# Performance work log

Measured on AMD Instinct MI355X. Metric: run time of the kernel, lower is better.

The kernel has to match this reference:

```python
import jax, jax.numpy as jnp
import numpy as np
from jax import lax

IMG_H, IMG_W = 800.0, 800.0
REG_WEIGHTS = (10.0, 10.0, 5.0, 5.0)
SCORE_THRESH = 0.05
NMS_THRESH = 0.5
NUM_DETECTIONS = 100
MIN_SIZE = 1.0
BBOX_XFORM_CLIP = float(np.log(1000.0 / 16.0))


def setup_inputs() -> dict:
    key = jax.random.key(0)
    k1, k2, k3, k4 = jax.random.split(key, 4)
    N, C = 1000, 81
    class_logit = jax.random.normal(k1, (N, C), dtype=jnp.float32) * 2.0
    box_regression = jax.random.normal(k2, (N, C * 4), dtype=jnp.float32)
    # proposals: valid (x1,y1,x2,y2) boxes inside the 800x800 image
    ctr = jax.random.uniform(k3, (N, 2), dtype=jnp.float32) * 800.0
    wh = jax.random.uniform(k4, (N, 2), dtype=jnp.float32) * 200.0 + 8.0
    x1y1 = jnp.clip(ctr - 0.5 * wh, 0.0, 800.0)
    x2y2 = jnp.clip(ctr + 0.5 * wh, 0.0, 800.0)
    proposal = jnp.concatenate([x1y1, x2y2], axis=1)
    return dict(class_logit=class_logit, box_regression=box_regression, proposal=proposal)


def decode_boxes(deltas, boxes):
    # deltas: [..., 4] (dx,dy,dw,dh); boxes: [..., 4] (x1,y1,x2,y2)
    wx, wy, ww, wh = REG_WEIGHTS
    widths = boxes[..., 2] - boxes[..., 0]
    heights = boxes[..., 3] - boxes[..., 1]
    ctr_x = boxes[..., 0] + 0.5 * widths
    ctr_y = boxes[..., 1] + 0.5 * heights
    dx = deltas[..., 0] / wx
    dy = deltas[..., 1] / wy
    dw = jnp.minimum(deltas[..., 2] / ww, BBOX_XFORM_CLIP)
    dh = jnp.minimum(deltas[..., 3] / wh, BBOX_XFORM_CLIP)
    pcx = dx * widths + ctr_x
    pcy = dy * heights + ctr_y
    pw = jnp.exp(dw) * widths
    ph = jnp.exp(dh) * heights
    return jnp.stack([pcx - 0.5 * pw, pcy - 0.5 * ph, pcx + 0.5 * pw, pcy + 0.5 * ph], axis=-1)


def pairwise_iou(b):
    # b: [N, 4] -> [N, N]
    area = (b[:, 2] - b[:, 0]) * (b[:, 3] - b[:, 1])
    lt = jnp.maximum(b[:, None, :2], b[None, :, :2])
    rb = jnp.minimum(b[:, None, 2:], b[None, :, 2:])
    wh = jnp.clip(rb - lt, 0.0)
    inter = wh[..., 0] * wh[..., 1]
    return inter / (area[:, None] + area[None, :] - inter + 1e-9)


def nms_one_class(boxes, scores):
    # boxes: [N, 4]; scores: [N] with invalid entries masked to -1.
    # Exact greedy NMS: sort by score desc, suppress IoU > NMS_THRESH.
    N = boxes.shape[0]
    order = jnp.argsort(-scores)
    b = boxes[order]
    s = scores[order]
    iou = pairwise_iou(b)
    valid = s > -0.5

    def body(carry, xs):
        keep, i = carry
        row, v = xs
        suppressed = jnp.any(keep & (row > NMS_THRESH))
        keep = keep.at[i].set(v & jnp.logical_not(suppressed))
        return (keep, i + 1), None

    (keep, _), _ = lax.scan(body, (jnp.zeros((N,), bool), jnp.int32(0)), (iou, valid))
    s_kept = jnp.where(keep, s, -1.0)
    top_s, top_i = lax.top_k(s_kept, NUM_DETECTIONS)  # kept are already score-sorted
    out_valid = top_s > -0.5
    out_boxes = jnp.where(out_valid[:, None], b[top_i], 0.0)
    out_scores = jnp.where(out_valid, top_s, 0.0)
    return out_boxes, out_scores, out_valid


def reference(class_logit, box_regression, proposal):
    N, C = class_logit.shape
    pred_score = jax.nn.softmax(class_logit, axis=-1)           # [N, C]
    deltas = box_regression.reshape(N, C, 4)
    boxes = decode_boxes(deltas[:, 1:, :], proposal[:, None, :])  # [N, C-1, 4]
    # clip to image (process_box)
    boxes = jnp.stack([
        jnp.clip(boxes[..., 0], 0.0, IMG_W),
        jnp.clip(boxes[..., 1], 0.0, IMG_H),
        jnp.clip(boxes[..., 2], 0.0, IMG_W),
        jnp.clip(boxes[..., 3], 0.0, IMG_H),
    ], axis=-1)
    w = boxes[..., 2] - boxes[..., 0]
    h = boxes[..., 3] - boxes[..., 1]
    score_fg = pred_score[:, 1:]                                 # [N, C-1]
    valid = (score_fg >= SCORE_THRESH) & (w >= MIN_SIZE) & (h >= MIN_SIZE)
    scores_m = jnp.where(valid, score_fg, -1.0)
    boxes_c = jnp.transpose(boxes, (1, 0, 2))                    # [C-1, N, 4]
    scores_c = scores_m.T                                        # [C-1, N]
    out_boxes, out_scores, out_valid = jax.vmap(nms_one_class)(boxes_c, scores_c)
    labels = jnp.broadcast_to(jnp.arange(1, C, dtype=jnp.int32)[:, None], out_scores.shape)
    labels = jnp.where(out_valid, labels, 0)
    # padded per-class detections: boxes [C-1, D, 4], scores/labels/valid [C-1, D]
    return out_boxes, out_scores, labels, out_valid
```

## Files before the change

### kernel.cpp

```cpp
#include <hip/hip_runtime.h>
#include <math.h>

#define N_PROP   1000
#define C_ALL    81
#define N_FG     80
#define TOPK     100
#define CAP      1024
#define IMG_WH   800.0f
#define SCORE_TH 0.05f
#define NMS_TH   0.5f
#define MIN_SZ   1.0f
#define BBOX_CLIP 4.135166556742356f

typedef unsigned long long u64;

__global__ __launch_bounds__(256) void softmax_stats_kernel(
    const float* __restrict__ logits,
    float* __restrict__ smax,
    float* __restrict__ ssum)
{
    const int wave = threadIdx.x >> 6;
    const int lane = threadIdx.x & 63;
    const int n = blockIdx.x * 4 + wave;
    if (n >= N_PROP) return;
    const float* row = logits + n * C_ALL;

    float v1 = row[lane];
    float v2 = (lane < C_ALL - 64) ? row[64 + lane] : 0.f;

    float m = (lane < C_ALL - 64) ? fmaxf(v1, v2) : v1;
    #pragma unroll
    for (int off = 32; off >= 1; off >>= 1)
        m = fmaxf(m, __shfl_xor(m, off, 64));

    float s = expf(v1 - m) + ((lane < C_ALL - 64) ? expf(v2 - m) : 0.0f);
    #pragma unroll
    for (int off = 32; off >= 1; off >>= 1)
        s += __shfl_xor(s, off, 64);

    if (lane == 0) { smax[n] = m; ssum[n] = s; }
}

__global__ __launch_bounds__(256) void roihead_kernel(
    const float* __restrict__ logits,
    const float* __restrict__ boxreg,
    const float* __restrict__ prop,
    const float* __restrict__ smax,
    const float* __restrict__ ssum,
    float* __restrict__ out)
{
    __shared__ u64   s_key[CAP];
    __shared__ float cx1[CAP], cy1[CAP], cx2[CAP], cy2[CAP], car[CAP];
    __shared__ float sx1[CAP], sy1[CAP], sx2[CAP], sy2[CAP], sar[CAP];
    __shared__ u64   s_mask[256 * 4];
    __shared__ u64   s_keep[4];
    __shared__ unsigned char s_rem[CAP];
    __shared__ int   s_cnt, s_emit;

    const int c   = blockIdx.x;
    const int tid = threadIdx.x;
    const int col = c + 1;

    const int OFF_SCORES = N_FG * TOPK * 4;
    const int OFF_LABELS = OFF_SCORES + N_FG * TOPK;
    const int OFF_VALID  = OFF_LABELS + N_FG * TOPK;

    for (int t = tid; t < TOPK * 4; t += 256) out[c * TOPK * 4 + t] = 0.0f;
    for (int t = tid; t < TOPK; t += 256) {
        out[OFF_SCORES + c * TOPK + t] = 0.0f;
        out[OFF_LABELS + c * TOPK + t] = 0.0f;
        out[OFF_VALID  + c * TOPK + t] = 0.0f;
    }
    if (tid == 0) { s_cnt = 0; s_emit = 0; }
    __syncthreads();

    for (int n = tid; n < N_PROP; n += 256) {
        float score = expf(logits[n * C_ALL + col] - smax[n]) / ssum[n];

        float4 p = *(const float4*)(prop + n * 4);
        float w  = p.z - p.x;
        float h  = p.w - p.y;
        float pcx0 = p.x + 0.5f * w;
        float pcy0 = p.y + 0.5f * h;

        float4 d = *(const float4*)(boxreg + n * (C_ALL * 4) + col * 4);
        float dx = d.x / 10.0f;
        float dy = d.y / 10.0f;
        float dw = fminf(d.z / 5.0f, BBOX_CLIP);
        float dh = fminf(d.w / 5.0f, BBOX_CLIP);

        float pcx = dx * w + pcx0;
        float pcy = dy * h + pcy0;
        float pw  = expf(dw) * w;
        float ph  = expf(dh) * h;

        float x1 = fminf(fmaxf(pcx - 0.5f * pw, 0.0f), IMG_WH);
        float y1 = fminf(fmaxf(pcy - 0.5f * ph, 0.0f), IMG_WH);
        float x2 = fminf(fmaxf(pcx + 0.5f * pw, 0.0f), IMG_WH);
        float y2 = fminf(fmaxf(pcy + 0.5f * ph, 0.0f), IMG_WH);

        float bw = x2 - x1;
        float bh = y2 - y1;
        if (score >= SCORE_TH && bw >= MIN_SZ && bh >= MIN_SZ) {
            int slot = atomicAdd(&s_cnt, 1);
            unsigned int fb = __float_as_uint(score);
            s_key[slot] = ((u64)fb << 20) | ((u64)(1023 - n) << 10) | (u64)slot;
            cx1[slot] = x1; cy1[slot] = y1; cx2[slot] = x2; cy2[slot] = y2;
            car[slot] = bw * bh;
        }
    }
    __syncthreads();

    const int V = s_cnt;
    if (V == 0) return;

    int VP2 = 1; while (VP2 < V) VP2 <<= 1;
    for (int t = V + tid; t < VP2; t += 256) s_key[t] = 0ull;
    __syncthreads();

    for (int k = 2; k <= VP2; k <<= 1) {
        for (int j = k >> 1; j > 0; j >>= 1) {
            for (int i = tid; i < VP2; i += 256) {
                int ixj = i ^ j;
                if (ixj > i) {
                    u64 a = s_key[i], b = s_key[ixj];
                    bool dir = ((i & k) == 0);
                    if ((b > a) == dir) { s_key[i] = b; s_key[ixj] = a; }
                }
            }
            __syncthreads();
        }
    }

    for (int t = tid; t < V; t += 256) {
        int slot = (int)(s_key[t] & 1023u);
        sx1[t] = cx1[slot]; sy1[t] = cy1[slot];
        sx2[t] = cx2[slot]; sy2[t] = cy2[slot];
        sar[t] = car[slot];
    }
    __syncthreads();

    if (V <= 256) {
        const int BW = (V + 63) >> 6;
        for (int i = tid; i < V; i += 256) {
            float x1i = sx1[i], y1i = sy1[i], x2i = sx2[i], y2i = sy2[i];
            float ai  = sar[i];
            for (int w = 0; w < BW; ++w) {
                u64 mrow = 0;
                int j0 = w << 6;
                int j1 = min(V, j0 + 64);
                for (int j = max(j0, i + 1); j < j1; ++j) {
                    float lx = fmaxf(x1i, sx1[j]);
                    float ly = fmaxf(y1i, sy1[j]);
                    float rx = fminf(x2i, sx2[j]);
                    float ry = fminf(y2i, sy2[j]);
                    float iw = fmaxf(rx - lx, 0.0f);
                    float ih = fmaxf(ry - ly, 0.0f);
                    float inter = iw * ih;
                    float iou = inter / (ai + sar[j] - inter + 1e-9f);
                    if (iou > NMS_TH) mrow |= 1ull << (j - j0);
                }
                s_mask[(i << 2) + w] = mrow;
            }
        }
        __syncthreads();

        if (tid == 0) {
            u64 r0 = 0, r1 = 0, r2 = 0, r3 = 0;
            u64 k0 = 0, k1 = 0, k2 = 0, k3 = 0;
            int kept = 0;
            for (int i = 0; i < V; ++i) {
                int w = i >> 6;
                u64 bit = 1ull << (i & 63);
                u64 rw = (w == 0) ? r0 : (w == 1) ? r1 : (w == 2) ? r2 : r3;
                if (rw & bit) continue;
                if (w == 0) k0 |= bit; else if (w == 1) k1 |= bit;
                else if (w == 2) k2 |= bit; else k3 |= bit;
                if (++kept >= TOPK) break;
                const u64* mr = &s_mask[i << 2];
                r0 |= mr[0];
                if (BW > 1) r1 |= mr[1];
                if (BW > 2) r2 |= mr[2];
                if (BW > 3) r3 |= mr[3];
            }
            s_keep[0] = k0; s_keep[1] = k1; s_keep[2] = k2; s_keep[3] = k3;
        }
        __syncthreads();

        u64 kw0 = s_keep[0], kw1 = s_keep[1], kw2 = s_keep[2], kw3 = s_keep[3];
        for (int t = tid; t < V; t += 256) {
            int w = t >> 6;
            u64 kw = (w == 0) ? kw0 : (w == 1) ? kw1 : (w == 2) ? kw2 : kw3;
            if (!((kw >> (t & 63)) & 1ull)) continue;
            int rank = 0;
            if (w > 0) rank += __popcll(kw0);
            if (w > 1) rank += __popcll(kw1);
            if (w > 2) rank += __popcll(kw2);
            rank += __popcll(kw & ((1ull << (t & 63)) - 1ull));
            if (rank < TOPK) {
                float score = __uint_as_float((unsigned int)(s_key[t] >> 20));
                out[(c * TOPK + rank) * 4 + 0] = sx1[t];
                out[(c * TOPK + rank) * 4 + 1] = sy1[t];
                out[(c * TOPK + rank) * 4 + 2] = sx2[t];
                out[(c * TOPK + rank) * 4 + 3] = sy2[t];
                out[OFF_SCORES + c * TOPK + rank] = score;
                out[OFF_LABELS + c * TOPK + rank] = (float)col;
                out[OFF_VALID  + c * TOPK + rank] = 1.0f;
            }
        }
    } else {
        for (int t = tid; t < V; t += 256) s_rem[t] = 0;
        __syncthreads();
        for (int i = 0; i < V; ++i) {
            if (s_rem[i]) continue;
            if (tid == 0) {
                int k = s_emit;
                if (k < TOPK) {
                    float score = __uint_as_float((unsigned int)(s_key[i] >> 20));
                    out[(c * TOPK + k) * 4 + 0] = sx1[i];
                    out[(c * TOPK + k) * 4 + 1] = sy1[i];
                    out[(c * TOPK + k) * 4 + 2] = sx2[i];
                    out[(c * TOPK + k) * 4 + 3] = sy2[i];
                    out[OFF_SCORES + c * TOPK + k] = score;
                    out[OFF_LABELS + c * TOPK + k] = (float)col;
                    out[OFF_VALID  + c * TOPK + k] = 1.0f;
                }
                s_emit = k + 1;
            }
            float x1i = sx1[i], y1i = sy1[i], x2i = sx2[i], y2i = sy2[i];
            float ai  = sar[i];
            for (int jj = i + 1 + tid; jj < V; jj += 256) {
                if (s_rem[jj]) continue;
                float lx = fmaxf(x1i, sx1[jj]);
                float ly = fmaxf(y1i, sy1[jj]);
                float rx = fminf(x2i, sx2[jj]);
                float ry = fminf(y2i, sy2[jj]);
                float iw = fmaxf(rx - lx, 0.0f);
                float ih = fmaxf(ry - ly, 0.0f);
                float inter = iw * ih;
                float iou = inter / (ai + sar[jj] - inter + 1e-9f);
                if (iou > NMS_TH) s_rem[jj] = 1;
            }
            __syncthreads();
            if (s_emit >= TOPK) break;
        }
    }
}

extern "C" void kernel_launch(void* const* d_in, const int* in_sizes, int n_in,
                              void* d_out, int out_size, void* d_ws, size_t ws_size,
                              hipStream_t stream) {
    const float* class_logit = (const float*)d_in[0];
    const float* box_reg     = (const float*)d_in[1];
    const float* proposal    = (const float*)d_in[2];
    float* out = (float*)d_out;

    float* ws   = (float*)d_ws;
    float* smax = ws;
    float* ssum = smax + N_PROP;

    softmax_stats_kernel<<<(N_PROP + 3) / 4, 256, 0, stream>>>(class_logit, smax, ssum);
    roihead_kernel<<<N_FG, 256, 0, stream>>>(class_logit, box_reg, proposal,
                                             smax, ssum, out);
}
```

Baseline: 92.81 us.

## Replace bitonic sort with rank sort and add single-wave NMS path

```diff
diff --git a/kernel.cpp b/kernel.cpp
--- a/kernel.cpp
+++ b/kernel.cpp
@@ -16,8 +16,7 @@
 
 __global__ __launch_bounds__(256) void softmax_stats_kernel(
     const float* __restrict__ logits,
-    float* __restrict__ smax,
-    float* __restrict__ ssum)
+    float2* __restrict__ stats)
 {
     const int wave = threadIdx.x >> 6;
     const int lane = threadIdx.x & 63;
@@ -38,19 +37,19 @@
     for (int off = 32; off >= 1; off >>= 1)
         s += __shfl_xor(s, off, 64);
 
-    if (lane == 0) { smax[n] = m; ssum[n] = s; }
+    if (lane == 0) stats[n] = make_float2(m, s);
 }
 
 __global__ __launch_bounds__(256) void roihead_kernel(
     const float* __restrict__ logits,
     const float* __restrict__ boxreg,
     const float* __restrict__ prop,
-    const float* __restrict__ smax,
-    const float* __restrict__ ssum,
+    const float2* __restrict__ stats,
     float* __restrict__ out)
 {
     __shared__ u64   s_key[CAP];
     __shared__ float cx1[CAP], cy1[CAP], cx2[CAP], cy2[CAP], car[CAP];
+    __shared__ u64   s_skey[CAP];
     __shared__ float sx1[CAP], sy1[CAP], sx2[CAP], sy2[CAP], sar[CAP];
     __shared__ u64   s_mask[256 * 4];
     __shared__ u64   s_keep[4];
@@ -75,7 +74,8 @@
     __syncthreads();
 
     for (int n = tid; n < N_PROP; n += 256) {
-        float score = expf(logits[n * C_ALL + col] - smax[n]) / ssum[n];
+        float2 ms = stats[n];
+        float score = expf(logits[n * C_ALL + col] - ms.x) / ms.y;
 
         float4 p = *(const float4*)(prop + n * 4);
         float w  = p.z - p.x;
@@ -114,33 +114,68 @@
     const int V = s_cnt;
     if (V == 0) return;
 
-    int VP2 = 1; while (VP2 < V) VP2 <<= 1;
-    for (int t = V + tid; t < VP2; t += 256) s_key[t] = 0ull;
+    for (int t = tid; t < V; t += 256) {
+        u64 myk = s_key[t];
+        int rank = 0;
+        for (int j = 0; j < V; ++j) rank += (s_key[j] > myk) ? 1 : 0;
+        s_skey[rank] = myk;
+        sx1[rank] = cx1[t]; sy1[rank] = cy1[t];
+        sx2[rank] = cx2[t]; sy2[rank] = cy2[t];
+        sar[rank] = car[t];
+    }
     __syncthreads();
 
-    for (int k = 2; k <= VP2; k <<= 1) {
-        for (int j = k >> 1; j > 0; j >>= 1) {
-            for (int i = tid; i < VP2; i += 256) {
-                int ixj = i ^ j;
-                if (ixj > i) {
-                    u64 a = s_key[i], b = s_key[ixj];
-                    bool dir = ((i & k) == 0);
-                    if ((b > a) == dir) { s_key[i] = b; s_key[ixj] = a; }
-                }
-            }
-            __syncthreads();
-        }
-    }
-
-    for (int t = tid; t < V; t += 256) {
-        int slot = (int)(s_key[t] & 1023u);
-        sx1[t] = cx1[slot]; sy1[t] = cy1[slot];
-        sx2[t] = cx2[slot]; sy2[t] = cy2[slot];
-        sar[t] = car[slot];
-    }
-    __syncthreads();
-
-    if (V <= 256) {
+    if (V <= 64) {
+        if (tid < 64) {
+            const int lane = tid;
+            bool act = lane < V;
+            float bx1 = 0.f, by1 = 0.f, bx2 = 0.f, by2 = 0.f, bar = 0.f;
+            if (act) {
+                bx1 = sx1[lane]; by1 = sy1[lane];
+                bx2 = sx2[lane]; by2 = sy2[lane];
+                bar = sar[lane];
+            }
+            u64 myrow = 0;
+            for (int i = 0; i < V; ++i) {
+                float ix1 = __shfl(bx1, i, 64);
+                float iy1 = __shfl(by1, i, 64);
+                float ix2 = __shfl(bx2, i, 64);
+                float iy2 = __shfl(by2, i, 64);
+                float iar = __shfl(bar, i, 64);
+                float lx = fmaxf(ix1, bx1);
+                float ly = fmaxf(iy1, by1);
+                float rx = fminf(ix2, bx2);
+                float ry = fminf(iy2, by2);
+                float iw = fmaxf(rx - lx, 0.0f);
+                float ih = fmaxf(ry - ly, 0.0f);
+                float inter = iw * ih;
+                float iou = inter / (iar + bar - inter + 1e-9f);
+                u64 bal = __ballot(act && (iou > NMS_TH));
+                if (lane == i) {
+                    u64 upper = (i == 63) ? 0ull : ~((1ull << (i + 1)) - 1ull);
+                    myrow = bal & upper;
+                }
+            }
+            u64 S = 0, K = 0;
+            for (int i = 0; i < V; ++i) {
+                if (!((S >> i) & 1ull)) {
+                    K |= 1ull << i;
+                    S |= __shfl(myrow, i, 64);
+                }
+            }
+            if (act && ((K >> lane) & 1ull)) {
+                int rank = __popcll(K & ((1ull << lane) - 1ull));
+                float score = __uint_as_float((unsigned int)(s_skey[lane] >> 20));
+                out[(c * TOPK + rank) * 4 + 0] = bx1;
+                out[(c * TOPK + rank) * 4 + 1] = by1;
+                out[(c * TOPK + rank) * 4 + 2] = bx2;
+                out[(c * TOPK + rank) * 4 + 3] = by2;
+                out[OFF_SCORES + c * TOPK + rank] = score;
+                out[OFF_LABELS + c * TOPK + rank] = (float)col;
+                out[OFF_VALID  + c * TOPK + rank] = 1.0f;
+            }
+        }
+    } else if (V <= 256) {
         const int BW = (V + 63) >> 6;
         for (int i = tid; i < V; i += 256) {
             float x1i = sx1[i], y1i = sy1[i], x2i = sx2[i], y2i = sy2[i];
@@ -198,7 +233,7 @@
             if (w > 2) rank += __popcll(kw2);
             rank += __popcll(kw & ((1ull << (t & 63)) - 1ull));
             if (rank < TOPK) {
-                float score = __uint_as_float((unsigned int)(s_key[t] >> 20));
+                float score = __uint_as_float((unsigned int)(s_skey[t] >> 20));
                 out[(c * TOPK + rank) * 4 + 0] = sx1[t];
                 out[(c * TOPK + rank) * 4 + 1] = sy1[t];
                 out[(c * TOPK + rank) * 4 + 2] = sx2[t];
@@ -216,7 +251,7 @@
             if (tid == 0) {
                 int k = s_emit;
                 if (k < TOPK) {
-                    float score = __uint_as_float((unsigned int)(s_key[i] >> 20));
+                    float score = __uint_as_float((unsigned int)(s_skey[i] >> 20));
                     out[(c * TOPK + k) * 4 + 0] = sx1[i];
                     out[(c * TOPK + k) * 4 + 1] = sy1[i];
                     out[(c * TOPK + k) * 4 + 2] = sx2[i];
@@ -255,11 +290,9 @@
     const float* proposal    = (const float*)d_in[2];
     float* out = (float*)d_out;
 
-    float* ws   = (float*)d_ws;
-    float* smax = ws;
-    float* ssum = smax + N_PROP;
-
-    softmax_stats_kernel<<<(N_PROP + 3) / 4, 256, 0, stream>>>(class_logit, smax, ssum);
+    float2* stats = (float2*)d_ws;
+
+    softmax_stats_kernel<<<(N_PROP + 3) / 4, 256, 0, stream>>>(class_logit, stats);
     roihead_kernel<<<N_FG, 256, 0, stream>>>(class_logit, box_reg, proposal,
-                                             smax, ssum, out);
+                                             stats, out);
 }
```

Measured after the change: 87.88 us. 1.06x faster.
